# Kernel tuning notes

Hardware: AMD Instinct MI355X
Metric: run time of the kernel (lower is better)

Reference implementation:

```python
import jax, jax.numpy as jnp
import numpy as np

N_NODES, N_EDGES, N_GRAPHS, D = 32768, 49152, 1024, 64


def setup_inputs() -> dict:
    key = jax.random.key(0)
    ks = jax.random.split(key, 24)
    p = lambda k, shape, s=0.1: jax.random.normal(k, shape, dtype=jnp.float32) * s
    return dict(
        x=jax.random.normal(ks[0], (N_NODES, 14), dtype=jnp.float32),
        edge_index=jax.random.randint(ks[1], (2, N_EDGES), 0, N_NODES),
        edge_attr=jax.random.uniform(ks[2], (N_EDGES, 4), dtype=jnp.float32),
        batch=jnp.sort(jax.random.randint(ks[3], (N_NODES,), 0, N_GRAPHS)),
        lin0_W=p(ks[4], (D, 14)), lin0_b=p(ks[5], (D,)),
        e1_W=p(ks[6], (128, 4)), e1_b=p(ks[7], (128,)),
        e2_W=p(ks[8], (D * D, 128), 0.02), e2_b=p(ks[9], (D * D,), 0.02),
        root_W=p(ks[10], (D, D)), conv_b=p(ks[11], (D,)),
        gru_Wih=p(ks[12], (3 * D, D)), gru_Whh=p(ks[13], (3 * D, D)),
        gru_bih=p(ks[14], (3 * D,)), gru_bhh=p(ks[15], (3 * D,)),
        lstm_Wih=p(ks[16], (4 * D, 2 * D)), lstm_Whh=p(ks[17], (4 * D, D)),
        lstm_bih=p(ks[18], (4 * D,)), lstm_bhh=p(ks[19], (4 * D,)),
        fc1_W=p(ks[20], (128, 2 * D)), fc1_b=p(ks[21], (128,)),
        fc2_W=p(ks[22], (1, 128)), fc2_b=p(ks[23], (1,)),
    )


def reference(x, edge_index, edge_attr, batch,
              lin0_W, lin0_b, e1_W, e1_b, e2_W, e2_b, root_W, conv_b,
              gru_Wih, gru_Whh, gru_bih, gru_bhh,
              lstm_Wih, lstm_Whh, lstm_bih, lstm_bhh,
              fc1_W, fc1_b, fc2_W, fc2_b):
    N, B = x.shape[0], N_GRAPHS
    src, dst = edge_index[0], edge_index[1]

    out = jax.nn.relu(x @ lin0_W.T + lin0_b)            # [N, D]
    h = out                                             # GRU hidden (num_layers=1)

    # Edge-conditioned weights: edge_attr is constant across the 3 iterations,
    # so compute the edge MLP once (identical math to re-running it).
    W = jax.nn.relu(edge_attr @ e1_W.T + e1_b) @ e2_W.T + e2_b
    W = W.reshape(-1, D, D)                             # [E, D, D]
    cnt = jnp.maximum(
        jax.ops.segment_sum(jnp.ones((src.shape[0],), x.dtype), dst, num_segments=N), 1.0)

    for _ in range(3):
        # NNConv (aggr='mean'): gather -> per-edge matmul -> scatter-mean -> root + bias
        msg = jnp.einsum('ei,eio->eo', out[src], W)     # [E, D]
        agg = jax.ops.segment_sum(msg, dst, num_segments=N) / cnt[:, None]
        m = jax.nn.relu(agg + out @ root_W + conv_b)
        # GRU cell (seq_len=1)
        gi = m @ gru_Wih.T + gru_bih
        gh = h @ gru_Whh.T + gru_bhh
        ir, iz, inn = jnp.split(gi, 3, -1)
        hr, hz, hn = jnp.split(gh, 3, -1)
        r = jax.nn.sigmoid(ir + hr)
        z = jax.nn.sigmoid(iz + hz)
        n = jnp.tanh(inn + r * hn)
        h = (1.0 - z) * n + z * h
        out = h

    # Set2Set pooling, 3 processing steps, LSTM(2D -> D)
    q_star = jnp.zeros((B, 2 * D), x.dtype)
    hl = jnp.zeros((B, D), x.dtype)
    cl = jnp.zeros((B, D), x.dtype)
    for _ in range(3):
        g = q_star @ lstm_Wih.T + lstm_bih + hl @ lstm_Whh.T + lstm_bhh
        i_, f_, g_, o_ = jnp.split(g, 4, -1)
        cl = jax.nn.sigmoid(f_) * cl + jax.nn.sigmoid(i_) * jnp.tanh(g_)
        hl = jax.nn.sigmoid(o_) * jnp.tanh(cl)
        q = hl                                          # [B, D]
        e = jnp.sum(out * q[batch], -1)                 # [N]
        mx = jax.ops.segment_max(e, batch, num_segments=B)
        ex = jnp.exp(e - mx[batch])
        den = jax.ops.segment_sum(ex, batch, num_segments=B)
        a = ex / den[batch]                             # segment softmax
        r_read = jax.ops.segment_sum(a[:, None] * out, batch, num_segments=B)
        q_star = jnp.concatenate([q, r_read], -1)       # [B, 2D]

    hid = jax.nn.relu(q_star @ fc1_W.T + fc1_b)
    return hid @ fc2_W.T + fc2_b                        # [B, 1]
```

## Files before the change

### kernel.cpp

```cpp
#include <hip/hip_runtime.h>
#include <math.h>

#define NN_ 32768
#define NE_ 49152
#define NG_ 1024

typedef short bh8 __attribute__((ext_vector_type(8)));
typedef float f32x4 __attribute__((ext_vector_type(4)));

__device__ __forceinline__ unsigned short f2bfu(float f) {
    union { float f; unsigned int i; } x; x.f = f;
    unsigned int u = x.i;
    u += 0x7FFFu + ((u >> 16) & 1u);
    return (unsigned short)(u >> 16);
}
__device__ __forceinline__ float sigm(float x) { return 1.f / (1.f + expf(-x)); }

__global__ void MPNN_78632261256134_kernel() {}

__global__ void k_init(float* cnt, float* qstar, float* aggb) {
    int i = blockIdx.x * 256 + threadIdx.x;
    if (i < NN_) cnt[i] = 0.f;
    int j = i - NN_;
    if (j >= 0 && j < NG_ * 256) qstar[j] = 0.f;
    int k = i - NN_ - NG_ * 256;
    if (k >= 0 && k < NN_ * 64) aggb[k] = 0.f;
}

__global__ void k_lin0(const float* x, const float* W, const float* b, float* node) {
    int g = blockIdx.x * 256 + threadIdx.x;
    int n = g >> 6, d = g & 63;
    const float* xr = x + n * 14;
    const float* wr = W + d * 14;
    float acc = b[d];
    for (int i = 0; i < 14; i++) acc += xr[i] * wr[i];
    node[g] = fmaxf(acc, 0.f);
}

__global__ void k_cnt(const int* dst, float* cnt) {
    int e = blockIdx.x * 256 + threadIdx.x;
    if (e < NE_) atomicAdd(&cnt[dst[e]], 1.0f);
}

__global__ void k_tw(const float* gWih, const float* gWhh, float* WihT, float* WhhT,
                     const float* lWih, const float* lWhh, float* WihT2, float* WhhT2) {
    int t = blockIdx.x * 256 + threadIdx.x;
    if (t < 12288) {
        int gr = t >> 6, i = t & 63; WihT[i * 192 + gr] = gWih[t];
    } else if (t < 24576) {
        int u = t - 12288; int gr = u >> 6, i = u & 63; WhhT[i * 192 + gr] = gWhh[u];
    } else if (t < 57344) {
        int u = t - 24576; int r = u >> 7, c = u & 127; WihT2[c * 256 + r] = lWih[u];
    } else if (t < 73728) {
        int u = t - 57344; int r = u >> 6, c = u & 63; WhhT2[c * 256 + r] = lWhh[u];
    }
}

__global__ void k_bhat3(const float* e2W, unsigned short* Bhat3) {
    int idx = blockIdx.x * 256 + threadIdx.x;
    if (idx >= 64 * 4 * 4 * 64 * 8) return;
    int j = idx & 7, lane = (idx >> 3) & 63, t = (idx >> 9) & 3, w = (idx >> 11) & 3, s = idx >> 13;
    int row = s * 64 + w * 16 + (lane & 15);
    int k = t * 32 + (lane >> 4) * 8 + j;
    Bhat3[idx] = f2bfu(e2W[row * 128 + k]);
}

__global__ __launch_bounds__(256) void k_he(const float* __restrict__ ea,
                                            const float* __restrict__ e1W,
                                            const float* __restrict__ e1b,
                                            unsigned short* __restrict__ Hhat) {
    int tid = threadIdx.x;
    int lane = tid & 63, sub = tid >> 6;
    int gi = blockIdx.x * 4 + sub;
    int etile = gi >> 2, t = gi & 3;
    int e = etile * 16 + (lane & 15), quad = lane >> 4;
    const float* ar = ea + (size_t)e * 4;
    float a0 = ar[0], a1 = ar[1], a2 = ar[2], a3 = ar[3];
    union { unsigned short u[8]; uint4 q; } o;
#pragma unroll
    for (int j = 0; j < 8; j++) {
        int c = t * 32 + quad * 8 + j;
        const float* wr = e1W + c * 4;
        float h = e1b[c] + a0 * wr[0] + a1 * wr[1] + a2 * wr[2] + a3 * wr[3];
        o.u[j] = f2bfu(fmaxf(h, 0.f));
    }
    *(uint4*)(Hhat + (size_t)gi * 512 + lane * 8) = o.q;
}

#define PS(S) (((S) + soff) & 63)

#define LDB(B, S) {                                                                       \
        const unsigned short* _p = Bhat3 + (size_t)PS(S) * 8192 + w * 2048 + lane * 8;    \
        (B)[0] = *(const bh8*)(const void*)(_p);                                          \
        (B)[1] = *(const bh8*)(const void*)(_p + 512);                                    \
        (B)[2] = *(const bh8*)(const void*)(_p + 1024);                                   \
        (B)[3] = *(const bh8*)(const void*)(_p + 1536); }

#define LDXV(XV, S) {                                                                     \
        int sp_ = PS(S);                                                                  \
        _Pragma("unroll")                                                                 \
        for (int mt_ = 0; mt_ < 4; mt_++)                                                 \
            (XV)[mt_] = *(const f32x4*)(const void*)(xs + sp_ * 68 + mt_ * 16 + quad * 4); }

#define LDBB(BB, S) (BB) = e2b[PS(S) * 64 + w * 16 + mrow];

#define MFMA16(ACC, B) {                                                                  \
        __builtin_amdgcn_s_setprio(1);                                                    \
        _Pragma("unroll")                                                                 \
        for (int t_ = 0; t_ < 4; t_++) {                                                  \
            _Pragma("unroll")                                                             \
            for (int mt_ = 0; mt_ < 4; mt_++)                                             \
                (ACC)[mt_] = __builtin_amdgcn_mfma_f32_16x16x32_bf16(                     \
                    af[mt_][t_], (B)[t_], (t_ == 0) ? z4 : (ACC)[mt_], 0, 0, 0);          \
        }                                                                                 \
        __builtin_amdgcn_s_setprio(0); }

#define CONSUME(ACC, XV, BB) {                                                            \
        _Pragma("unroll")                                                                 \
        for (int mt_ = 0; mt_ < 4; mt_++) {                                               \
            _Pragma("unroll")                                                             \
            for (int r_ = 0; r_ < 4; r_++)                                                \
                msg[mt_][r_] += (XV)[mt_][r_] * ((ACC)[mt_][r_] + (BB));                  \
        } }

__global__ __launch_bounds__(256, 2) void k_convr(const float* __restrict__ node,
                                                  const unsigned short* __restrict__ Hhat,
                                                  const unsigned short* __restrict__ Bhat3,
                                                  const float* __restrict__ e2b,
                                                  const int* __restrict__ src,
                                                  const int* __restrict__ dst,
                                                  float* __restrict__ agg) {
    __shared__ __align__(16) float xs[64 * 68];
    __shared__ int dst_s[64];

    const int tid = threadIdx.x;
    const int eb = blockIdx.x * 64;
    const int lane = tid & 63, w = tid >> 6;
    const int quad = lane >> 4, mrow = lane & 15;
    const int soff = (blockIdx.x * 37) & 63;

    {
        int r = tid >> 2, c = tid & 3;
        int s = src[eb + r];
        const float* nr = node + (size_t)s * 64 + c * 16;
#pragma unroll
        for (int j = 0; j < 16; j++) xs[(c * 16 + j) * 68 + r] = nr[j];
        if (tid < 64) dst_s[tid] = dst[eb + tid];
    }

    bh8 af[4][4];
#pragma unroll
    for (int mt = 0; mt < 4; mt++)
#pragma unroll
        for (int t = 0; t < 4; t++)
            af[mt][t] = *(const bh8*)(const void*)(
                Hhat + (size_t)(((eb >> 4) + mt) * 4 + t) * 512 + lane * 8);
    __syncthreads();

    const f32x4 z4 = {0.f, 0.f, 0.f, 0.f};
    f32x4 msg[4];
#pragma unroll
    for (int mt = 0; mt < 4; mt++) msg[mt] = z4;

    bh8 b0[4], b1[4];
    f32x4 xvA[4], xvB[4];
    f32x4 accA[4], accB[4];
    float bbA, bbB;

    LDB(b0, 0)
    LDB(b1, 1)
    LDXV(xvA, 0)
    LDBB(bbA, 0)
    MFMA16(accA, b0)
    LDB(b0, 2)

#pragma unroll 1
    for (int s = 0; s < 62; s += 2) {
        MFMA16(accB, b1)
        LDB(b1, s + 3)
        LDXV(xvB, s + 1)
        LDBB(bbB, s + 1)
        CONSUME(accA, xvA, bbA)
        MFMA16(accA, b0)
        LDB(b0, (s + 4) & 63)
        LDXV(xvA, s + 2)
        LDBB(bbA, s + 2)
        CONSUME(accB, xvB, bbB)
    }
    MFMA16(accB, b1)
    CONSUME(accA, xvA, bbA)
    LDXV(xvB, 63)
    LDBB(bbB, 63)
    CONSUME(accB, xvB, bbB)

#pragma unroll
    for (int mt = 0; mt < 4; mt++)
#pragma unroll
        for (int r = 0; r < 4; r++)
            atomicAdd(agg + (size_t)dst_s[mt * 16 + quad * 4 + r] * 64 + w * 16 + mrow,
                      msg[mt][r]);
}

__global__ __launch_bounds__(256) void k_mgru(float* __restrict__ agg,
                                              const float* __restrict__ cnt,
                                              const float* __restrict__ node,
                                              const float* __restrict__ rootW,
                                              const float* __restrict__ convb,
                                              const float* __restrict__ WihT,
                                              const float* __restrict__ WhhT,
                                              const float* __restrict__ bih,
                                              const float* __restrict__ bhh,
                                              float* __restrict__ hOut) {
    __shared__ __align__(16) float hsT[64][20];
    __shared__ __align__(16) float msT[64][20];
    const int tid = threadIdx.x;
    const int d = tid & 63, sub = tid >> 6;
    const int nb = blockIdx.x * 16;
    const int r0 = sub * 4;
    const int off = (blockIdx.x * 37) & 63;

    {
        f32x4 hv;
#pragma unroll
        for (int j = 0; j < 4; j++)
            hv[j] = node[(size_t)(nb + r0 + j) * 64 + d];
        *(f32x4*)&hsT[d][r0] = hv;
    }
    __syncthreads();

    {
        f32x4 root = {0.f, 0.f, 0.f, 0.f};
        for (int ii = 0; ii < 64; ii++) {
            int i = (ii + off) & 63;
            float wv = rootW[i * 64 + d];
            f32x4 h4 = *(const f32x4*)&hsT[i][r0];
#pragma unroll
            for (int j = 0; j < 4; j++) root[j] += h4[j] * wv;
        }
        float cb = convb[d];
        f32x4 mval;
#pragma unroll
        for (int j = 0; j < 4; j++) {
            int n = nb + r0 + j;
            float inv = 1.f / fmaxf(cnt[n], 1.f);
            float av = agg[(size_t)n * 64 + d];
            agg[(size_t)n * 64 + d] = 0.f;
            mval[j] = fmaxf(av * inv + cb + root[j], 0.f);
        }
        *(f32x4*)&msT[d][r0] = mval;
    }
    __syncthreads();

    float ir[4], iz[4], in_[4], hr[4], hz[4], hn[4];
    {
        float bi0 = bih[d], bi1 = bih[64 + d], bi2 = bih[128 + d];
        float bh0 = bhh[d], bh1 = bhh[64 + d], bh2 = bhh[128 + d];
#pragma unroll
        for (int j = 0; j < 4; j++) {
            ir[j] = bi0; iz[j] = bi1; in_[j] = bi2;
            hr[j] = bh0; hz[j] = bh1; hn[j] = bh2;
        }
    }
    for (int ii = 0; ii < 64; ii++) {
        int i = (ii + off) & 63;
        float wi0 = WihT[i * 192 + d];
        float wi1 = WihT[i * 192 + 64 + d];
        float wi2 = WihT[i * 192 + 128 + d];
        float wh0 = WhhT[i * 192 + d];
        float wh1 = WhhT[i * 192 + 64 + d];
        float wh2 = WhhT[i * 192 + 128 + d];
        f32x4 m4 = *(const f32x4*)&msT[i][r0];
        f32x4 h4 = *(const f32x4*)&hsT[i][r0];
#pragma unroll
        for (int j = 0; j < 4; j++) {
            ir[j] += m4[j] * wi0; iz[j] += m4[j] * wi1; in_[j] += m4[j] * wi2;
            hr[j] += h4[j] * wh0; hz[j] += h4[j] * wh1; hn[j] += h4[j] * wh2;
        }
    }
    f32x4 hold = *(const f32x4*)&hsT[d][r0];
#pragma unroll
    for (int j = 0; j < 4; j++) {
        float r = sigm(ir[j] + hr[j]);
        float z = sigm(iz[j] + hz[j]);
        float nn = tanhf(in_[j] + r * hn[j]);
        hOut[(size_t)(nb + r0 + j) * 64 + d] = (1.f - z) * nn + z * hold[j];
    }
}

__global__ __launch_bounds__(64) void k_s2s(const float* __restrict__ node,
                                            const int* __restrict__ batch,
                                            const float* __restrict__ WihT2,
                                            const float* __restrict__ WhhT2,
                                            const float* __restrict__ bih,
                                            const float* __restrict__ bhh,
                                            float* __restrict__ cl,
                                            float* __restrict__ hl,
                                            float* __restrict__ qstar) {
    __shared__ float qvs[128];
    __shared__ float hls[64];
    const int b = blockIdx.x, lane = threadIdx.x;
    const int joff = (b * 37) & 127;
    const int koff = (b * 37) & 63;

    qvs[lane] = qstar[(size_t)b * 128 + lane];
    qvs[64 + lane] = qstar[(size_t)b * 128 + 64 + lane];
    hls[lane] = hl[(size_t)b * 64 + lane];
    __syncthreads();

    float acc0 = bih[lane] + bhh[lane];
    float acc1 = bih[64 + lane] + bhh[64 + lane];
    float acc2 = bih[128 + lane] + bhh[128 + lane];
    float acc3 = bih[192 + lane] + bhh[192 + lane];
    for (int jj = 0; jj < 128; jj++) {
        int j = (jj + joff) & 127;
        float qj = qvs[j];
        const float* wr = WihT2 + (size_t)j * 256;
        acc0 += qj * wr[lane];
        acc1 += qj * wr[64 + lane];
        acc2 += qj * wr[128 + lane];
        acc3 += qj * wr[192 + lane];
    }
    for (int jj = 0; jj < 64; jj++) {
        int j = (jj + koff) & 63;
        float hj = hls[j];
        const float* wr = WhhT2 + (size_t)j * 256;
        acc0 += hj * wr[lane];
        acc1 += hj * wr[64 + lane];
        acc2 += hj * wr[128 + lane];
        acc3 += hj * wr[192 + lane];
    }
    float c = sigm(acc1) * cl[(size_t)b * 64 + lane] + sigm(acc0) * tanhf(acc2);
    cl[(size_t)b * 64 + lane] = c;
    float q = sigm(acc3) * tanhf(c);
    hl[(size_t)b * 64 + lane] = q;

    int lo = 0, hi = NN_;
    while (lo < hi) { int mid = (lo + hi) >> 1; if (batch[mid] < b) lo = mid + 1; else hi = mid; }
    int start = lo;
    lo = start; hi = NN_;
    while (lo < hi) { int mid = (lo + hi) >> 1; if (batch[mid] < b + 1) lo = mid + 1; else hi = mid; }
    int end = lo;

    float r_acc = 0.f, m_run = -1e30f, l_run = 0.f;
    for (int n = start; n < end; n++) {
        float nv = node[(size_t)n * 64 + lane];
        float p = nv * q;
#pragma unroll
        for (int o = 32; o > 0; o >>= 1) p += __shfl_xor(p, o);
        float m_new = fmaxf(m_run, p);
        float sc = expf(m_run - m_new);
        float wgt = expf(p - m_new);
        l_run = l_run * sc + wgt;
        r_acc = r_acc * sc + wgt * nv;
        m_run = m_new;
    }
    qstar[(size_t)b * 128 + lane] = q;
    qstar[(size_t)b * 128 + 64 + lane] = (end > start) ? r_acc / l_run : 0.f;
}

__global__ void k_fc(const float* qstar, const float* W1, const float* b1,
                     const float* W2, const float* b2, float* out) {
    __shared__ float hid[128];
    int b = blockIdx.x; int t = threadIdx.x;
    const float* qr = qstar + (size_t)b * 128;
    float acc = b1[t];
    const float* wr = W1 + (size_t)t * 128;
    for (int k = 0; k < 128; k++) acc += qr[k] * wr[k];
    hid[t] = fmaxf(acc, 0.f);
    __syncthreads();
    if (t < 64) {
        float s = hid[t] * W2[t] + hid[t + 64] * W2[t + 64];
        for (int o = 32; o > 0; o >>= 1) s += __shfl_xor(s, o);
        if (t == 0) out[b] = s + b2[0];
    }
}

extern "C" void kernel_launch(void* const* d_in, const int* in_sizes, int n_in,
                              void* d_out, int out_size, void* d_ws, size_t ws_size,
                              hipStream_t stream) {
    const float* x     = (const float*)d_in[0];
    const int*   ei    = (const int*)d_in[1];
    const float* ea    = (const float*)d_in[2];
    const int*   batch = (const int*)d_in[3];
    const float* lin0W = (const float*)d_in[4];
    const float* lin0b = (const float*)d_in[5];
    const float* e1W   = (const float*)d_in[6];
    const float* e1b   = (const float*)d_in[7];
    const float* e2W   = (const float*)d_in[8];
    const float* e2b   = (const float*)d_in[9];
    const float* rootW = (const float*)d_in[10];
    const float* convb = (const float*)d_in[11];
    const float* gWih  = (const float*)d_in[12];
    const float* gWhh  = (const float*)d_in[13];
    const float* gbih  = (const float*)d_in[14];
    const float* gbhh  = (const float*)d_in[15];
    const float* lWih  = (const float*)d_in[16];
    const float* lWhh  = (const float*)d_in[17];
    const float* lbih  = (const float*)d_in[18];
    const float* lbhh  = (const float*)d_in[19];
    const float* fc1W  = (const float*)d_in[20];
    const float* fc1b  = (const float*)d_in[21];
    const float* fc2W  = (const float*)d_in[22];
    const float* fc2b  = (const float*)d_in[23];
    const int* src = ei;
    const int* dst = ei + NE_;

    char* p = (char*)d_ws;
    auto alloc = [&](size_t bytes) -> char* {
        char* r = p; p += (bytes + 255) & ~(size_t)255; return r;
    };
    unsigned short* Bhat3 = (unsigned short*)alloc((size_t)524288 * 2);
    unsigned short* Hhat  = (unsigned short*)alloc((size_t)NE_ * 128 * 2);
    float* nodeA  = (float*)alloc((size_t)NN_ * 64 * 4);
    float* nodeB  = (float*)alloc((size_t)NN_ * 64 * 4);
    float* aggb   = (float*)alloc((size_t)NN_ * 64 * 4);
    float* cnt    = (float*)alloc((size_t)NN_ * 4);
    float* WihT   = (float*)alloc(192 * 64 * 4);
    float* WhhT   = (float*)alloc(192 * 64 * 4);
    float* WihT2  = (float*)alloc(256 * 128 * 4);
    float* WhhT2  = (float*)alloc(256 * 64 * 4);
    float* qstar  = (float*)alloc((size_t)NG_ * 128 * 4);
    float* hl     = (float*)alloc((size_t)NG_ * 64 * 4);
    float* clb    = (float*)alloc((size_t)NG_ * 64 * 4);

    k_init<<<(NN_ + NG_ * 256 + NN_ * 64 + 255) / 256, 256, 0, stream>>>(cnt, qstar, aggb);
    k_lin0<<<NN_ * 64 / 256, 256, 0, stream>>>(x, lin0W, lin0b, nodeA);
    k_cnt<<<NE_ / 256, 256, 0, stream>>>(dst, cnt);
    k_tw<<<288, 256, 0, stream>>>(gWih, gWhh, WihT, WhhT, lWih, lWhh, WihT2, WhhT2);
    k_bhat3<<<524288 / 256, 256, 0, stream>>>(e2W, Bhat3);
    k_he<<<NE_ / 16, 256, 0, stream>>>(ea, e1W, e1b, Hhat);

    float* curF = nodeA; float* nxtF = nodeB;
    for (int it = 0; it < 3; it++) {
        k_convr<<<NE_ / 64, 256, 0, stream>>>(curF, Hhat, Bhat3, e2b, src, dst, aggb);
        k_mgru<<<NN_ / 16, 256, 0, stream>>>(aggb, cnt, curF, rootW, convb,
                                             WihT, WhhT, gbih, gbhh, nxtF);
        float* tf = curF; curF = nxtF; nxtF = tf;
    }

    for (int s = 0; s < 3; s++)
        k_s2s<<<NG_, 64, 0, stream>>>(curF, batch, WihT2, WhhT2, lbih, lbhh, clb, hl, qstar);
    k_fc<<<NG_, 128, 0, stream>>>(qstar, fc1W, fc1b, fc2W, fc2b, (float*)d_out);
}
```

Before: 514.8 us.

## Replace atomic scatter-mean with CSR-sorted edges and deterministic per-node gather

Builds a CSR layout of edges by destination (degree count, single-block scan, atomic scatter into a permutation) so each conv pass writes per-edge messages contiguously and the GRU kernel sums them per node, with no float atomics and no agg zeroing. Also precomputes graph boundaries so Set2Set skips binary searches, and unrolls the online-softmax loop four nodes at a time. The cost is extra setup kernels, a serial single-block scan, and a larger message buffer that is written and read back each iteration.

```diff
diff --git a/kernel.cpp b/kernel.cpp
--- a/kernel.cpp
+++ b/kernel.cpp
@@ -18,13 +18,11 @@
 
 __global__ void MPNN_78632261256134_kernel() {}
 
-__global__ void k_init(float* cnt, float* qstar, float* aggb) {
+__global__ void k_init(int* deg, float* qstar) {
     int i = blockIdx.x * 256 + threadIdx.x;
-    if (i < NN_) cnt[i] = 0.f;
+    if (i < NN_) deg[i] = 0;
     int j = i - NN_;
     if (j >= 0 && j < NG_ * 256) qstar[j] = 0.f;
-    int k = i - NN_ - NG_ * 256;
-    if (k >= 0 && k < NN_ * 64) aggb[k] = 0.f;
 }
 
 __global__ void k_lin0(const float* x, const float* W, const float* b, float* node) {
@@ -37,9 +35,52 @@
     node[g] = fmaxf(acc, 0.f);
 }
 
-__global__ void k_cnt(const int* dst, float* cnt) {
+__global__ void k_cnt(const int* dst, int* deg) {
     int e = blockIdx.x * 256 + threadIdx.x;
-    if (e < NE_) atomicAdd(&cnt[dst[e]], 1.0f);
+    if (e < NE_) atomicAdd(&deg[dst[e]], 1);
+}
+
+__global__ __launch_bounds__(256) void k_scan(const int* __restrict__ deg,
+                                              int* __restrict__ offs,
+                                              int* __restrict__ head) {
+    __shared__ int wsum[4];
+    int tid = threadIdx.x;
+    int base = tid * 128;
+    int s = 0;
+#pragma unroll 1
+    for (int i = 0; i < 128; i++) s += deg[base + i];
+    int v = s, sc = s;
+    for (int o = 1; o < 64; o <<= 1) { int u = __shfl_up(sc, o); if ((tid & 63) >= o) sc += u; }
+    if ((tid & 63) == 63) wsum[tid >> 6] = sc;
+    __syncthreads();
+    int wpre = 0;
+    for (int i = 0; i < (tid >> 6); i++) wpre += wsum[i];
+    int run = sc + wpre - v;
+#pragma unroll 1
+    for (int i = 0; i < 128; i++) {
+        int dv = deg[base + i];
+        offs[base + i] = run; head[base + i] = run;
+        run += dv;
+    }
+    if (tid == 255) offs[NN_] = run;
+}
+
+__global__ void k_scatter(const int* __restrict__ dst, int* __restrict__ head,
+                          int* __restrict__ perm) {
+    int e = blockIdx.x * 256 + threadIdx.x;
+    if (e < NE_) { int p = atomicAdd(&head[dst[e]], 1); perm[p] = e; }
+}
+
+__global__ void k_gbnd(const int* __restrict__ batch, int* __restrict__ gb) {
+    int n = blockIdx.x * 256 + threadIdx.x;
+    if (n >= NN_) return;
+    int b = batch[n];
+    if (n == 0) { for (int g = 0; g <= b; g++) gb[g] = 0; }
+    else {
+        int pb = batch[n - 1];
+        for (int g = pb + 1; g <= b; g++) gb[g] = n;
+    }
+    if (n == NN_ - 1) { for (int g = b + 1; g <= NG_; g++) gb[g] = NN_; }
 }
 
 __global__ void k_tw(const float* gWih, const float* gWhh, float* WihT, float* WhhT,
@@ -68,13 +109,15 @@
 __global__ __launch_bounds__(256) void k_he(const float* __restrict__ ea,
                                             const float* __restrict__ e1W,
                                             const float* __restrict__ e1b,
+                                            const int* __restrict__ perm,
                                             unsigned short* __restrict__ Hhat) {
     int tid = threadIdx.x;
     int lane = tid & 63, sub = tid >> 6;
     int gi = blockIdx.x * 4 + sub;
     int etile = gi >> 2, t = gi & 3;
     int e = etile * 16 + (lane & 15), quad = lane >> 4;
-    const float* ar = ea + (size_t)e * 4;
+    int eo = perm[e];
+    const float* ar = ea + (size_t)eo * 4;
     float a0 = ar[0], a1 = ar[1], a2 = ar[2], a3 = ar[3];
     union { unsigned short u[8]; uint4 q; } o;
 #pragma unroll
@@ -120,7 +163,7 @@
         for (int mt_ = 0; mt_ < 4; mt_++) {                                               \
             _Pragma("unroll")                                                             \
             for (int r_ = 0; r_ < 4; r_++)                                                \
-                msg[mt_][r_] += (XV)[mt_][r_] * ((ACC)[mt_][r_] + (BB));                  \
+                msgv[mt_][r_] += (XV)[mt_][r_] * ((ACC)[mt_][r_] + (BB));                 \
         } }
 
 __global__ __launch_bounds__(256, 2) void k_convr(const float* __restrict__ node,
@@ -128,10 +171,9 @@
                                                   const unsigned short* __restrict__ Bhat3,
                                                   const float* __restrict__ e2b,
                                                   const int* __restrict__ src,
-                                                  const int* __restrict__ dst,
-                                                  float* __restrict__ agg) {
+                                                  const int* __restrict__ perm,
+                                                  float* __restrict__ msg) {
     __shared__ __align__(16) float xs[64 * 68];
-    __shared__ int dst_s[64];
 
     const int tid = threadIdx.x;
     const int eb = blockIdx.x * 64;
@@ -141,11 +183,10 @@
 
     {
         int r = tid >> 2, c = tid & 3;
-        int s = src[eb + r];
+        int s = src[perm[eb + r]];
         const float* nr = node + (size_t)s * 64 + c * 16;
 #pragma unroll
         for (int j = 0; j < 16; j++) xs[(c * 16 + j) * 68 + r] = nr[j];
-        if (tid < 64) dst_s[tid] = dst[eb + tid];
     }
 
     bh8 af[4][4];
@@ -158,9 +199,9 @@
     __syncthreads();
 
     const f32x4 z4 = {0.f, 0.f, 0.f, 0.f};
-    f32x4 msg[4];
-#pragma unroll
-    for (int mt = 0; mt < 4; mt++) msg[mt] = z4;
+    f32x4 msgv[4];
+#pragma unroll
+    for (int mt = 0; mt < 4; mt++) msgv[mt] = z4;
 
     bh8 b0[4], b1[4];
     f32x4 xvA[4], xvB[4];
@@ -197,12 +238,11 @@
     for (int mt = 0; mt < 4; mt++)
 #pragma unroll
         for (int r = 0; r < 4; r++)
-            atomicAdd(agg + (size_t)dst_s[mt * 16 + quad * 4 + r] * 64 + w * 16 + mrow,
-                      msg[mt][r]);
-}
-
-__global__ __launch_bounds__(256) void k_mgru(float* __restrict__ agg,
-                                              const float* __restrict__ cnt,
+            msg[(size_t)(eb + mt * 16 + quad * 4 + r) * 64 + w * 16 + mrow] = msgv[mt][r];
+}
+
+__global__ __launch_bounds__(256) void k_mgru(const float* __restrict__ msg,
+                                              const int* __restrict__ offs,
                                               const float* __restrict__ node,
                                               const float* __restrict__ rootW,
                                               const float* __restrict__ convb,
@@ -242,9 +282,10 @@
 #pragma unroll
         for (int j = 0; j < 4; j++) {
             int n = nb + r0 + j;
-            float inv = 1.f / fmaxf(cnt[n], 1.f);
-            float av = agg[(size_t)n * 64 + d];
-            agg[(size_t)n * 64 + d] = 0.f;
+            int o0 = offs[n], o1 = offs[n + 1];
+            float av = 0.f;
+            for (int t = o0; t < o1; t++) av += msg[(size_t)t * 64 + d];
+            float inv = 1.f / fmaxf((float)(o1 - o0), 1.f);
             mval[j] = fmaxf(av * inv + cb + root[j], 0.f);
         }
         *(f32x4*)&msT[d][r0] = mval;
@@ -288,7 +329,7 @@
 }
 
 __global__ __launch_bounds__(64) void k_s2s(const float* __restrict__ node,
-                                            const int* __restrict__ batch,
+                                            const int* __restrict__ gb,
                                             const float* __restrict__ WihT2,
                                             const float* __restrict__ WhhT2,
                                             const float* __restrict__ bih,
@@ -334,15 +375,33 @@
     float q = sigm(acc3) * tanhf(c);
     hl[(size_t)b * 64 + lane] = q;
 
-    int lo = 0, hi = NN_;
-    while (lo < hi) { int mid = (lo + hi) >> 1; if (batch[mid] < b) lo = mid + 1; else hi = mid; }
-    int start = lo;
-    lo = start; hi = NN_;
-    while (lo < hi) { int mid = (lo + hi) >> 1; if (batch[mid] < b + 1) lo = mid + 1; else hi = mid; }
-    int end = lo;
+    const int start = gb[b], end = gb[b + 1];
 
     float r_acc = 0.f, m_run = -1e30f, l_run = 0.f;
-    for (int n = start; n < end; n++) {
+    int n = start;
+    for (; n + 3 < end; n += 4) {
+        float nv0 = node[(size_t)(n + 0) * 64 + lane];
+        float nv1 = node[(size_t)(n + 1) * 64 + lane];
+        float nv2 = node[(size_t)(n + 2) * 64 + lane];
+        float nv3 = node[(size_t)(n + 3) * 64 + lane];
+        float p0 = nv0 * q, p1 = nv1 * q, p2 = nv2 * q, p3 = nv3 * q;
+#pragma unroll
+        for (int o = 32; o > 0; o >>= 1) {
+            p0 += __shfl_xor(p0, o);
+            p1 += __shfl_xor(p1, o);
+            p2 += __shfl_xor(p2, o);
+            p3 += __shfl_xor(p3, o);
+        }
+        float mx = fmaxf(fmaxf(p0, p1), fmaxf(p2, p3));
+        float m_new = fmaxf(m_run, mx);
+        float sc = expf(m_run - m_new);
+        float w0 = expf(p0 - m_new), w1 = expf(p1 - m_new);
+        float w2 = expf(p2 - m_new), w3 = expf(p3 - m_new);
+        l_run = l_run * sc + ((w0 + w1) + (w2 + w3));
+        r_acc = r_acc * sc + ((w0 * nv0 + w1 * nv1) + (w2 * nv2 + w3 * nv3));
+        m_run = m_new;
+    }
+    for (; n < end; n++) {
         float nv = node[(size_t)n * 64 + lane];
         float p = nv * q;
 #pragma unroll
@@ -413,8 +472,12 @@
     unsigned short* Hhat  = (unsigned short*)alloc((size_t)NE_ * 128 * 2);
     float* nodeA  = (float*)alloc((size_t)NN_ * 64 * 4);
     float* nodeB  = (float*)alloc((size_t)NN_ * 64 * 4);
-    float* aggb   = (float*)alloc((size_t)NN_ * 64 * 4);
-    float* cnt    = (float*)alloc((size_t)NN_ * 4);
+    float* msgb   = (float*)alloc((size_t)NE_ * 64 * 4);
+    int*   deg    = (int*)alloc((size_t)NN_ * 4);
+    int*   offs   = (int*)alloc((size_t)(NN_ + 1) * 4);
+    int*   head   = (int*)alloc((size_t)NN_ * 4);
+    int*   perm   = (int*)alloc((size_t)NE_ * 4);
+    int*   gb     = (int*)alloc((size_t)(NG_ + 1) * 4);
     float* WihT   = (float*)alloc(192 * 64 * 4);
     float* WhhT   = (float*)alloc(192 * 64 * 4);
     float* WihT2  = (float*)alloc(256 * 128 * 4);
@@ -423,22 +486,25 @@
     float* hl     = (float*)alloc((size_t)NG_ * 64 * 4);
     float* clb    = (float*)alloc((size_t)NG_ * 64 * 4);
 
-    k_init<<<(NN_ + NG_ * 256 + NN_ * 64 + 255) / 256, 256, 0, stream>>>(cnt, qstar, aggb);
+    k_init<<<(NN_ + NG_ * 256 + 255) / 256, 256, 0, stream>>>(deg, qstar);
     k_lin0<<<NN_ * 64 / 256, 256, 0, stream>>>(x, lin0W, lin0b, nodeA);
-    k_cnt<<<NE_ / 256, 256, 0, stream>>>(dst, cnt);
+    k_cnt<<<NE_ / 256, 256, 0, stream>>>(dst, deg);
+    k_scan<<<1, 256, 0, stream>>>(deg, offs, head);
+    k_scatter<<<NE_ / 256, 256, 0, stream>>>(dst, head, perm);
+    k_gbnd<<<NN_ / 256, 256, 0, stream>>>(batch, gb);
     k_tw<<<288, 256, 0, stream>>>(gWih, gWhh, WihT, WhhT, lWih, lWhh, WihT2, WhhT2);
     k_bhat3<<<524288 / 256, 256, 0, stream>>>(e2W, Bhat3);
-    k_he<<<NE_ / 16, 256, 0, stream>>>(ea, e1W, e1b, Hhat);
+    k_he<<<NE_ / 16, 256, 0, stream>>>(ea, e1W, e1b, perm, Hhat);
 
     float* curF = nodeA; float* nxtF = nodeB;
     for (int it = 0; it < 3; it++) {
-        k_convr<<<NE_ / 64, 256, 0, stream>>>(curF, Hhat, Bhat3, e2b, src, dst, aggb);
-        k_mgru<<<NN_ / 16, 256, 0, stream>>>(aggb, cnt, curF, rootW, convb,
+        k_convr<<<NE_ / 64, 256, 0, stream>>>(curF, Hhat, Bhat3, e2b, src, perm, msgb);
+        k_mgru<<<NN_ / 16, 256, 0, stream>>>(msgb, offs, curF, rootW, convb,
                                              WihT, WhhT, gbih, gbhh, nxtF);
         float* tf = curF; curF = nxtF; nxtF = tf;
     }
 
     for (int s = 0; s < 3; s++)
-        k_s2s<<<NG_, 64, 0, stream>>>(curF, batch, WihT2, WhhT2, lbih, lbhh, clb, hl, qstar);
+        k_s2s<<<NG_, 64, 0, stream>>>(curF, gb, WihT2, WhhT2, lbih, lbhh, clb, hl, qstar);
     k_fc<<<NG_, 128, 0, stream>>>(qstar, fc1W, fc1b, fc2W, fc2b, (float*)d_out);
 }
```

Result: slower. 715.7 us (+39.0%).
